# Kernel tuning notes

Hardware: AMD Instinct MI355X
Metric: run time of the kernel (lower is better)

Reference implementation:

```python
import math
import jax, jax.numpy as jnp
import numpy as np

DIM = 4096
N_HEADS = 32
N_KV_HEADS = 8
HEAD_DIM = DIM // N_HEADS          # 128
N_REP = N_HEADS // N_KV_HEADS      # 4
B, T = 2, 2048
MAX_SEQ = 2048
ROPE_THETA = 500000.0


def _rope_tables(seq_len, head_dim, theta):
    inv = 1.0 / (theta ** (np.arange(0, head_dim, 2, dtype=np.float32) / head_dim))
    t = np.arange(seq_len, dtype=np.float32)
    ang = np.outer(t, inv)                      # [T, head_dim/2]
    return jnp.asarray(np.cos(ang)), jnp.asarray(np.sin(ang))


def setup_inputs() -> dict:
    key = jax.random.key(0)
    ks = jax.random.split(key, 6)
    scale = 0.02
    x = jax.random.normal(ks[0], (B, T, DIM), dtype=jnp.float32)
    wq = jax.random.normal(ks[1], (N_HEADS * HEAD_DIM, DIM), dtype=jnp.float32) * scale
    wk = jax.random.normal(ks[2], (N_KV_HEADS * HEAD_DIM, DIM), dtype=jnp.float32) * scale
    wv = jax.random.normal(ks[3], (N_KV_HEADS * HEAD_DIM, DIM), dtype=jnp.float32) * scale
    wo = jax.random.normal(ks[4], (DIM, N_HEADS * HEAD_DIM), dtype=jnp.float32) * scale
    freqs_cos, freqs_sin = _rope_tables(T, HEAD_DIM, ROPE_THETA)
    cache_k = jnp.zeros((B, MAX_SEQ, N_KV_HEADS, HEAD_DIM), dtype=jnp.float32)
    cache_v = jnp.zeros((B, MAX_SEQ, N_KV_HEADS, HEAD_DIM), dtype=jnp.float32)
    mask = jnp.zeros((T, T), dtype=jnp.float32)  # NOTE: unused by the original forward
    return {"x": x, "wq": wq, "wk": wk, "wv": wv, "wo": wo,
            "freqs_cos": freqs_cos, "freqs_sin": freqs_sin,
            "cache_k": cache_k, "cache_v": cache_v,
            "mask": mask, "start_pos": 0}


def _apply_rope(t, cos, sin):
    # t: [B, T, H, hd]; even/odd interleaved pairs form complex numbers
    tr = t.reshape(*t.shape[:-1], HEAD_DIM // 2, 2)
    xr, xi = tr[..., 0], tr[..., 1]
    c = cos[None, :, None, :]
    s = sin[None, :, None, :]
    out_r = xr * c - xi * s
    out_i = xr * s + xi * c
    return jnp.stack([out_r, out_i], axis=-1).reshape(t.shape)


def reference(x, wq, wk, wv, wo, freqs_cos, freqs_sin, cache_k, cache_v, mask, start_pos):
    Bx, Tx, _ = x.shape
    q = (x @ wq.T).reshape(Bx, Tx, N_HEADS, HEAD_DIM)
    k = (x @ wk.T).reshape(Bx, Tx, N_KV_HEADS, HEAD_DIM)
    v = (x @ wv.T).reshape(Bx, Tx, N_KV_HEADS, HEAD_DIM)

    q = _apply_rope(q, freqs_cos, freqs_sin)
    k = _apply_rope(k, freqs_cos, freqs_sin)

    # KV-cache append (start_pos is a static Python int)
    cache_k = jax.lax.dynamic_update_slice(cache_k, k, (0, start_pos, 0, 0))
    cache_v = jax.lax.dynamic_update_slice(cache_v, v, (0, start_pos, 0, 0))
    S = start_pos + Tx

    # GQA expansion via torch-style .repeat (tiling: head h -> kv head h % n_kv)
    keys = jnp.tile(cache_k[:, :S], (1, 1, N_REP, 1))    # [B, S, H, hd]
    values = jnp.tile(cache_v[:, :S], (1, 1, N_REP, 1))  # [B, S, H, hd]

    scores = jnp.einsum('bthd,bshd->bhts', q, keys) / math.sqrt(HEAD_DIM)
    # NOTE: the original forward never adds `mask` — faithful unmasked softmax
    probs = jax.nn.softmax(scores, axis=-1)
    ctx = jnp.einsum('bhts,bshd->bthd', probs, values).reshape(Bx, Tx, N_HEADS * HEAD_DIM)
    return ctx @ wo.T
```

## Files before the change

### kernel.cpp

```cpp
#include <hip/hip_runtime.h>
#include <hip/hip_bf16.h>
#include <cstdint>


typedef short bf16x8 __attribute__((ext_vector_type(8)));
typedef float f32x4  __attribute__((ext_vector_type(4)));

__device__ __forceinline__ float b2f(unsigned short h) {
  union { uint32_t u; float f; } v; v.u = ((uint32_t)h) << 16; return v.f;
}
__device__ __forceinline__ unsigned short f2b(float f) {
  union { float f; uint32_t u; } v; v.f = f;
  uint32_t r = (v.u + 0x7FFFu + ((v.u >> 16) & 1u)) >> 16;
  return (unsigned short)r;
}

#define GLDS16(gp, lp)                                                        \
  __builtin_amdgcn_global_load_lds(                                           \
      (const __attribute__((address_space(1))) unsigned int*)(gp),            \
      (__attribute__((address_space(3))) unsigned int*)(lp), 16, 0, 0)

__global__ __launch_bounds__(256) void cast_f32_bf16(
    const float* __restrict__ in, unsigned short* __restrict__ out, int n4) {
  int i = blockIdx.x * 256 + threadIdx.x;
  if (i < n4) {
    float4 v = ((const float4*)in)[i];
    ushort4 o;
    o.x = f2b(v.x); o.y = f2b(v.y); o.z = f2b(v.z); o.w = f2b(v.w);
    ((ushort4*)out)[i] = o;
  }
}

__device__ __forceinline__ void stout(float* p, float v) { *p = v; }
__device__ __forceinline__ void stout(unsigned short* p, float v) { *p = f2b(v); }

template <typename OUT>
__global__ __launch_bounds__(256, 2) void gemm_bt(
    const unsigned short* __restrict__ A, const unsigned short* __restrict__ B,
    OUT* __restrict__ C, int M, int N, int K) {
  __shared__ __align__(16) unsigned short As[128][64];
  __shared__ __align__(16) unsigned short Bs[128][64];

  const int tid  = threadIdx.x;
  const int lane = tid & 63;
  const int wave = tid >> 6;
  const int col  = lane & 15;
  const int quad = lane >> 4;
  const int bm = blockIdx.y * 128;
  const int bn = blockIdx.x * 128;
  const int wm = (wave & 1) * 64;
  const int wn = (wave >> 1) * 64;

  f32x4 acc[4][4];
#pragma unroll
  for (int i = 0; i < 4; ++i)
#pragma unroll
    for (int j = 0; j < 4; ++j) acc[i][j] = (f32x4){0.f, 0.f, 0.f, 0.f};

  const int srow0  = tid >> 3;
  const int gchunk = (tid & 7) ^ ((tid >> 3) & 7);
  const unsigned short* Ag = A + (size_t)(bm + srow0) * K + gchunk * 8;
  const unsigned short* Bg = B + (size_t)(bn + srow0) * K + gchunk * 8;
  unsigned short* Al = &As[0][0] + tid * 8;
  unsigned short* Bl = &Bs[0][0] + tid * 8;

  for (int k0 = 0; k0 < K; k0 += 64) {
    __syncthreads();
#pragma unroll
    for (int r = 0; r < 4; ++r) {
      GLDS16(Ag + k0 + (size_t)r * 32 * K, Al + r * 2048);
      GLDS16(Bg + k0 + (size_t)r * 32 * K, Bl + r * 2048);
    }
    __syncthreads();
#pragma unroll
    for (int ks = 0; ks < 2; ++ks) {
      bf16x8 a[4], b[4];
      const int slot = ((ks * 4 + quad) ^ (col & 7)) * 8;
#pragma unroll
      for (int i = 0; i < 4; ++i)
        a[i] = *(const bf16x8*)&As[wm + i * 16 + col][slot];
#pragma unroll
      for (int j = 0; j < 4; ++j)
        b[j] = *(const bf16x8*)&Bs[wn + j * 16 + col][slot];
#pragma unroll
      for (int i = 0; i < 4; ++i)
#pragma unroll
        for (int j = 0; j < 4; ++j)
          acc[i][j] = __builtin_amdgcn_mfma_f32_16x16x32_bf16(a[i], b[j],
                                                              acc[i][j], 0, 0, 0);
    }
  }

#pragma unroll
  for (int i = 0; i < 4; ++i) {
    int row = bm + wm + i * 16 + quad * 4;
#pragma unroll
    for (int j = 0; j < 4; ++j) {
      int cc = bn + wn + j * 16 + col;
#pragma unroll
      for (int r2 = 0; r2 < 4; ++r2)
        stout(C + (size_t)(row + r2) * N + cc, acc[i][j][r2]);
    }
  }
}

__global__ __launch_bounds__(256) void rope_qk(
    unsigned short* __restrict__ qkv, const float* __restrict__ cosT,
    const float* __restrict__ sinT) {
  int idx = blockIdx.x * 256 + threadIdx.x;
  int m = idx / 2560;
  int p = idx - m * 2560;
  int head = p >> 6, i = p & 63;
  int t = m & 2047;
  unsigned short* ptr = qkv + (size_t)m * 6144 + head * 128 + i * 2;
  ushort2 xy = *(const ushort2*)ptr;
  float x = b2f(xy.x), y = b2f(xy.y);
  float c = cosT[t * 64 + i], s = sinT[t * 64 + i];
  ushort2 o;
  o.x = f2b(x * c - y * s);
  o.y = f2b(x * s + y * c);
  *(ushort2*)ptr = o;
}

__global__ __launch_bounds__(256) void transpose_v(
    const unsigned short* __restrict__ qkv, unsigned short* __restrict__ vt) {
  __shared__ unsigned short tile[64][72];
  int b = blockIdx.z >> 3, kvh = blockIdx.z & 7;
  int s0 = blockIdx.x * 64, d0 = blockIdx.y * 64;
  int tc = threadIdx.x & 63, tr = threadIdx.x >> 6;
#pragma unroll
  for (int r = 0; r < 16; ++r) {
    int row = r * 4 + tr;
    tile[row][tc] =
        qkv[(size_t)(b * 2048 + s0 + row) * 6144 + 5120 + kvh * 128 + d0 + tc];
  }
  __syncthreads();
#pragma unroll
  for (int r = 0; r < 16; ++r) {
    int drow = r * 4 + tr;
    vt[(size_t)((b * 8 + kvh) * 128 + d0 + drow) * 2048 + s0 + tc] =
        tile[tc][drow];
  }
}

__global__ __launch_bounds__(256, 2) void attn(
    const unsigned short* __restrict__ qkv, const unsigned short* __restrict__ vt,
    unsigned short* __restrict__ ctx) {
  constexpr int T = 2048, LD = 6144;
  const int qt = blockIdx.x, h = blockIdx.y, b = blockIdx.z;
  const int kvh = h & 7;
  const int tid = threadIdx.x, lane = tid & 63, wave = tid >> 6;
  const int col = lane & 15, quad = lane >> 4;

  __shared__ __align__(1024) char smem[51200];
  auto Qs = (unsigned short(*)[128][8])smem;
  auto Ks = (unsigned short(*)[128])smem;
  auto Vs = (unsigned short(*)[64])(smem + 16384);
  auto Ps = (unsigned short(*)[72])(smem + 32768);

  {
    const int row = tid & 127, kc0 = tid >> 7;
    const unsigned short* g =
        qkv + (size_t)(b * T + qt * 128 + row) * LD + h * 128 + kc0 * 8;
    unsigned short* l = &Qs[kc0][row][0];
#pragma unroll
    for (int r = 0; r < 8; ++r) GLDS16(g + r * 16, l + r * 2048);
  }
  __syncthreads();

  bf16x8 qf[2][4];
#pragma unroll
  for (int mi = 0; mi < 2; ++mi)
#pragma unroll
    for (int ks = 0; ks < 4; ++ks)
      qf[mi][ks] = *(const bf16x8*)&Qs[ks * 4 + quad][wave * 32 + mi * 16 + col][0];

  float mrow[2], lrow[2];
  f32x4 oacc[2][8];
#pragma unroll
  for (int mi = 0; mi < 2; ++mi) { mrow[mi] = -1e30f; lrow[mi] = 0.f; }
#pragma unroll
  for (int mi = 0; mi < 2; ++mi)
#pragma unroll
    for (int d = 0; d < 8; ++d) oacc[mi][d] = (f32x4){0.f, 0.f, 0.f, 0.f};

  const float scale = 0.08838834764831845f;
  const float l2e = 1.4426950408889634f;

  const int krow0 = tid >> 4;
  const int kgch  = (tid & 15) ^ ((tid >> 4) & 15);
  const int vrow0 = tid >> 3;
  const int vgch  = (tid & 7) ^ ((tid >> 3) & 7);
  unsigned short* Klin = &Ks[0][0] + tid * 8;
  unsigned short* Vlin = &Vs[0][0] + tid * 8;

  for (int s0 = 0; s0 < T; s0 += 64) {
    __syncthreads();
    {
      const unsigned short* g =
          qkv + (size_t)(b * T + s0 + krow0) * LD + 4096 + kvh * 128 + kgch * 8;
#pragma unroll
      for (int r = 0; r < 4; ++r)
        GLDS16(g + (size_t)r * 16 * LD, Klin + r * 2048);
      const unsigned short* gv =
          vt + (size_t)((b * 8 + kvh) * 128 + vrow0) * T + s0 + vgch * 8;
#pragma unroll
      for (int r = 0; r < 4; ++r)
        GLDS16(gv + (size_t)r * 32 * T, Vlin + r * 2048);
    }
    __syncthreads();

    f32x4 sacc[2][4];
#pragma unroll
    for (int mi = 0; mi < 2; ++mi)
#pragma unroll
      for (int j = 0; j < 4; ++j) sacc[mi][j] = (f32x4){0.f, 0.f, 0.f, 0.f};
#pragma unroll
    for (int ks = 0; ks < 4; ++ks) {
      bf16x8 ak[4];
#pragma unroll
      for (int j = 0; j < 4; ++j)
        ak[j] = *(const bf16x8*)&Ks[j * 16 + col][((ks * 4 + quad) ^ col) * 8];
#pragma unroll
      for (int mi = 0; mi < 2; ++mi)
#pragma unroll
        for (int j = 0; j < 4; ++j)
          sacc[mi][j] = __builtin_amdgcn_mfma_f32_16x16x32_bf16(
              ak[j], qf[mi][ks], sacc[mi][j], 0, 0, 0);
    }

#pragma unroll
    for (int mi = 0; mi < 2; ++mi) {
      const int q = wave * 32 + mi * 16 + col;
      float mx = sacc[mi][0][0];
#pragma unroll
      for (int j = 0; j < 4; ++j)
#pragma unroll
        for (int r = 0; r < 4; ++r) mx = fmaxf(mx, sacc[mi][j][r]);
      mx = fmaxf(mx, __shfl_xor(mx, 16));
      mx = fmaxf(mx, __shfl_xor(mx, 32));
      mx *= scale;
      float mold = mrow[mi];
      float mnew = fmaxf(mold, mx);
      float alpha = exp2f((mold - mnew) * l2e);
      mrow[mi] = mnew;
      float rsum = 0.f;
#pragma unroll
      for (int j = 0; j < 4; ++j) {
        ushort4 pk;
#pragma unroll
        for (int r = 0; r < 4; ++r) {
          float pv = exp2f((sacc[mi][j][r] * scale - mnew) * l2e);
          rsum += pv;
          ((unsigned short*)&pk)[r] = f2b(pv);
        }
        *(ushort4*)&Ps[q][j * 16 + quad * 4] = pk;
      }
      rsum += __shfl_xor(rsum, 16);
      rsum += __shfl_xor(rsum, 32);
      lrow[mi] = lrow[mi] * alpha + rsum;
#pragma unroll
      for (int di = 0; di < 8; ++di) {
#pragma unroll
        for (int r = 0; r < 4; ++r) oacc[mi][di][r] *= alpha;
      }
    }

#pragma unroll
    for (int mi = 0; mi < 2; ++mi) {
      const int q = wave * 32 + mi * 16 + col;
      bf16x8 bp[2];
      bp[0] = *(const bf16x8*)&Ps[q][quad * 8];
      bp[1] = *(const bf16x8*)&Ps[q][32 + quad * 8];
#pragma unroll
      for (int ks = 0; ks < 2; ++ks) {
#pragma unroll
        for (int di = 0; di < 8; ++di) {
          bf16x8 va = *(const bf16x8*)
              &Vs[di * 16 + col][(((ks * 4 + quad) ^ (col & 7))) * 8];
          oacc[mi][di] = __builtin_amdgcn_mfma_f32_16x16x32_bf16(
              va, bp[ks], oacc[mi][di], 0, 0, 0);
        }
      }
    }
  }

#pragma unroll
  for (int mi = 0; mi < 2; ++mi) {
    float inv = 1.0f / lrow[mi];
    int row = qt * 128 + wave * 32 + mi * 16 + col;
    unsigned short* cp = ctx + (size_t)(b * T + row) * 4096 + h * 128;
#pragma unroll
    for (int di = 0; di < 8; ++di)
#pragma unroll
      for (int r = 0; r < 4; ++r)
        cp[di * 16 + quad * 4 + r] = f2b(oacc[mi][di][r] * inv);
  }
}

extern "C" void kernel_launch(void* const* d_in, const int* in_sizes, int n_in,
                              void* d_out, int out_size, void* d_ws,
                              size_t ws_size, hipStream_t stream) {
  const float* x  = (const float*)d_in[0];
  const float* wq = (const float*)d_in[1];
  const float* wk = (const float*)d_in[2];
  const float* wv = (const float*)d_in[3];
  const float* wo = (const float*)d_in[4];
  const float* fc = (const float*)d_in[5];
  const float* fs = (const float*)d_in[6];
  float* out = (float*)d_out;

  char* ws = (char*)d_ws;
  unsigned short* xb  = (unsigned short*)(ws);
  unsigned short* wb  = (unsigned short*)(ws + 33554432);
  unsigned short* qkv = (unsigned short*)(ws + 33554432 + 50331648);
  unsigned short* vtp = (unsigned short*)(ws + 33554432 + 50331648 + 50331648);

  cast_f32_bf16<<<16384, 256, 0, stream>>>(x, xb, 4194304);
  cast_f32_bf16<<<16384, 256, 0, stream>>>(wq, wb, 4194304);
  cast_f32_bf16<<<4096, 256, 0, stream>>>(wk, wb + 16777216, 1048576);
  cast_f32_bf16<<<4096, 256, 0, stream>>>(wv, wb + 20971520, 1048576);

  dim3 g1(48, 32);
  gemm_bt<unsigned short><<<g1, 256, 0, stream>>>(xb, wb, qkv, 4096, 6144, 4096);

  cast_f32_bf16<<<16384, 256, 0, stream>>>(wo, wb, 4194304);

  rope_qk<<<40960, 256, 0, stream>>>(qkv, fc, fs);

  dim3 g2(32, 2, 16);
  transpose_v<<<g2, 256, 0, stream>>>(qkv, vtp);

  dim3 g3(16, 32, 2);
  attn<<<g3, 256, 0, stream>>>(qkv, vtp, xb);

  dim3 g4(32, 32);
  gemm_bt<float><<<g4, 256, 0, stream>>>(xb, wb, out, 4096, 4096, 4096);
}
```

Baseline: 847.9 us.

## Vectorize RoPE, use packed bf16 converts, fold softmax scale, reuse V fragments

RoPE now has each thread handle four rotation pairs with 16-byte loads and stores, and the grid shrinks to match. The attention softmax folds scale and log2e into a single multiply-subtract and packs probabilities with the hardware v_cvt_pk_bf16_f32 instruction. The PV loop is reordered so each V fragment read from LDS feeds both row tiles, halving V LDS reads. Output stores also use packed converts with 8-byte writes; the hardware convert may round differently from the manual round-to-nearest-even routine.

```diff
diff --git a/kernel.cpp b/kernel.cpp
--- a/kernel.cpp
+++ b/kernel.cpp
@@ -13,6 +13,17 @@
   union { float f; uint32_t u; } v; v.f = f;
   uint32_t r = (v.u + 0x7FFFu + ((v.u >> 16) & 1u)) >> 16;
   return (unsigned short)r;
+}
+__device__ __forceinline__ uint32_t cvt_pk_bf16(float lo, float hi) {
+  uint32_t r;
+  asm("v_cvt_pk_bf16_f32 %0, %1, %2" : "=v"(r) : "v"(lo), "v"(hi));
+  return r;
+}
+__device__ __forceinline__ float lo2f(uint32_t u) {
+  union { uint32_t u; float f; } w; w.u = u << 16; return w.f;
+}
+__device__ __forceinline__ float hi2f(uint32_t u) {
+  union { uint32_t u; float f; } w; w.u = u & 0xffff0000u; return w.f;
 }
 
 #define GLDS16(gp, lp)                                                        \
@@ -108,18 +119,24 @@
     unsigned short* __restrict__ qkv, const float* __restrict__ cosT,
     const float* __restrict__ sinT) {
   int idx = blockIdx.x * 256 + threadIdx.x;
-  int m = idx / 2560;
-  int p = idx - m * 2560;
-  int head = p >> 6, i = p & 63;
+  int m = idx / 640;
+  int p = idx - m * 640;
+  int head = p >> 4, i4 = p & 15;
   int t = m & 2047;
-  unsigned short* ptr = qkv + (size_t)m * 6144 + head * 128 + i * 2;
-  ushort2 xy = *(const ushort2*)ptr;
-  float x = b2f(xy.x), y = b2f(xy.y);
-  float c = cosT[t * 64 + i], s = sinT[t * 64 + i];
-  ushort2 o;
-  o.x = f2b(x * c - y * s);
-  o.y = f2b(x * s + y * c);
-  *(ushort2*)ptr = o;
+  unsigned short* ptr = qkv + (size_t)m * 6144 + head * 128 + i4 * 8;
+  uint4 v = *(const uint4*)ptr;
+  float4 c = *(const float4*)&cosT[t * 64 + i4 * 4];
+  float4 s = *(const float4*)&sinT[t * 64 + i4 * 4];
+  float x0 = lo2f(v.x), y0 = hi2f(v.x);
+  float x1 = lo2f(v.y), y1 = hi2f(v.y);
+  float x2 = lo2f(v.z), y2 = hi2f(v.z);
+  float x3 = lo2f(v.w), y3 = hi2f(v.w);
+  uint4 o;
+  o.x = cvt_pk_bf16(x0 * c.x - y0 * s.x, x0 * s.x + y0 * c.x);
+  o.y = cvt_pk_bf16(x1 * c.y - y1 * s.y, x1 * s.y + y1 * c.y);
+  o.z = cvt_pk_bf16(x2 * c.z - y2 * s.z, x2 * s.z + y2 * c.z);
+  o.w = cvt_pk_bf16(x3 * c.w - y3 * s.w, x3 * s.w + y3 * c.w);
+  *(uint4*)ptr = o;
 }
 
 __global__ __launch_bounds__(256) void transpose_v(
@@ -186,6 +203,7 @@
 
   const float scale = 0.08838834764831845f;
   const float l2e = 1.4426950408889634f;
+  const float c1 = scale * l2e;
 
   const int krow0 = tid >> 4;
   const int kgch  = (tid & 15) ^ ((tid >> 4) & 15);
@@ -244,17 +262,19 @@
       float mnew = fmaxf(mold, mx);
       float alpha = exp2f((mold - mnew) * l2e);
       mrow[mi] = mnew;
+      const float mml = mnew * l2e;
       float rsum = 0.f;
 #pragma unroll
       for (int j = 0; j < 4; ++j) {
-        ushort4 pk;
-#pragma unroll
-        for (int r = 0; r < 4; ++r) {
-          float pv = exp2f((sacc[mi][j][r] * scale - mnew) * l2e);
-          rsum += pv;
-          ((unsigned short*)&pk)[r] = f2b(pv);
-        }
-        *(ushort4*)&Ps[q][j * 16 + quad * 4] = pk;
+        float p0 = exp2f(sacc[mi][j][0] * c1 - mml);
+        float p1 = exp2f(sacc[mi][j][1] * c1 - mml);
+        float p2 = exp2f(sacc[mi][j][2] * c1 - mml);
+        float p3 = exp2f(sacc[mi][j][3] * c1 - mml);
+        rsum += (p0 + p1) + (p2 + p3);
+        uint2 pk;
+        pk.x = cvt_pk_bf16(p0, p1);
+        pk.y = cvt_pk_bf16(p2, p3);
+        *(uint2*)&Ps[q][j * 16 + quad * 4] = pk;
       }
       rsum += __shfl_xor(rsum, 16);
       rsum += __shfl_xor(rsum, 32);
@@ -266,21 +286,23 @@
       }
     }
 
+    bf16x8 bp[2][2];
 #pragma unroll
     for (int mi = 0; mi < 2; ++mi) {
       const int q = wave * 32 + mi * 16 + col;
-      bf16x8 bp[2];
-      bp[0] = *(const bf16x8*)&Ps[q][quad * 8];
-      bp[1] = *(const bf16x8*)&Ps[q][32 + quad * 8];
-#pragma unroll
-      for (int ks = 0; ks < 2; ++ks) {
-#pragma unroll
-        for (int di = 0; di < 8; ++di) {
-          bf16x8 va = *(const bf16x8*)
-              &Vs[di * 16 + col][(((ks * 4 + quad) ^ (col & 7))) * 8];
+      bp[mi][0] = *(const bf16x8*)&Ps[q][quad * 8];
+      bp[mi][1] = *(const bf16x8*)&Ps[q][32 + quad * 8];
+    }
+#pragma unroll
+    for (int ks = 0; ks < 2; ++ks) {
+#pragma unroll
+      for (int di = 0; di < 8; ++di) {
+        bf16x8 va = *(const bf16x8*)
+            &Vs[di * 16 + col][(((ks * 4 + quad) ^ (col & 7))) * 8];
+#pragma unroll
+        for (int mi = 0; mi < 2; ++mi)
           oacc[mi][di] = __builtin_amdgcn_mfma_f32_16x16x32_bf16(
-              va, bp[ks], oacc[mi][di], 0, 0, 0);
-        }
+              va, bp[mi][ks], oacc[mi][di], 0, 0, 0);
       }
     }
   }
@@ -291,10 +313,12 @@
     int row = qt * 128 + wave * 32 + mi * 16 + col;
     unsigned short* cp = ctx + (size_t)(b * T + row) * 4096 + h * 128;
 #pragma unroll
-    for (int di = 0; di < 8; ++di)
-#pragma unroll
-      for (int r = 0; r < 4; ++r)
-        cp[di * 16 + quad * 4 + r] = f2b(oacc[mi][di][r] * inv);
+    for (int di = 0; di < 8; ++di) {
+      uint2 o;
+      o.x = cvt_pk_bf16(oacc[mi][di][0] * inv, oacc[mi][di][1] * inv);
+      o.y = cvt_pk_bf16(oacc[mi][di][2] * inv, oacc[mi][di][3] * inv);
+      *(uint2*)(cp + di * 16 + quad * 4) = o;
+    }
   }
 }
 
@@ -326,7 +350,7 @@
 
   cast_f32_bf16<<<16384, 256, 0, stream>>>(wo, wb, 4194304);
 
-  rope_qk<<<40960, 256, 0, stream>>>(qkv, fc, fs);
+  rope_qk<<<10240, 256, 0, stream>>>(qkv, fc, fs);
 
   dim3 g2(32, 2, 16);
   transpose_v<<<g2, 256, 0, stream>>>(qkv, vtp);
```

New measurement: 821.3 us. 3.1% less time.
